# Kernel tuning notes

Measured on AMD Instinct MI355X. Metric: run time of the kernel, lower is better.

Reference implementation:

```python
import jax, jax.numpy as jnp
import numpy as np

D_MODEL = 2048
NUM_HEADS = 16
D_KV = D_MODEL // NUM_HEADS
THETA = 10000.0
N_LORA = 4
RANK = 16
BATCH = 2
SEQ = 2048


def setup_inputs() -> dict:
    key = jax.random.key(0)
    ks = jax.random.split(key, 16)
    s = 0.02
    inp = {
        'x': jax.random.normal(ks[0], (BATCH, SEQ, D_MODEL), jnp.float32),
        'lora_start_indices': jnp.sort(jax.random.randint(ks[1], (N_LORA,), 0, BATCH)),
        'Wq': jax.random.normal(ks[2], (D_MODEL, D_MODEL), jnp.float32) * s,
        'Aq': jax.random.normal(ks[3], (N_LORA, RANK, D_MODEL), jnp.float32) * s,
        'Bq': jax.random.normal(ks[4], (N_LORA, D_MODEL, RANK), jnp.float32) * s,
        'Wk': jax.random.normal(ks[5], (D_MODEL, D_MODEL), jnp.float32) * s,
        'Ak': jax.random.normal(ks[6], (N_LORA, RANK, D_MODEL), jnp.float32) * s,
        'Bk': jax.random.normal(ks[7], (N_LORA, D_MODEL, RANK), jnp.float32) * s,
        'Wv': jax.random.normal(ks[8], (D_MODEL, D_MODEL), jnp.float32) * s,
        'Av': jax.random.normal(ks[9], (N_LORA, RANK, D_MODEL), jnp.float32) * s,
        'Bv': jax.random.normal(ks[10], (N_LORA, D_MODEL, RANK), jnp.float32) * s,
        'Wo': jax.random.normal(ks[11], (D_MODEL, D_MODEL), jnp.float32) * s,
        'Ao': jax.random.normal(ks[12], (N_LORA, RANK, D_MODEL), jnp.float32) * s,
        'Bo': jax.random.normal(ks[13], (N_LORA, D_MODEL, RANK), jnp.float32) * s,
    }
    return inp


def _adapter_ids(starts, batch):
    # each batch row b uses the adapter whose start index is the last one <= b
    ids = jnp.searchsorted(starts, jnp.arange(batch), side='right') - 1
    return jnp.clip(ids, 0, starts.shape[0] - 1)


def _multilora(x, ids, W, A, B):
    # x: [b, s, d_in]; W: [d_out, d_in]; A: [L, r, d_in]; B: [L, d_out, r]
    base = jnp.einsum('bsd,od->bso', x, W)
    Ai, Bi = A[ids], B[ids]                       # [b, r, d_in], [b, d_out, r]
    low = jnp.einsum('bsd,brd->bsr', x, Ai)
    return base + jnp.einsum('bsr,bor->bso', low, Bi)


def _rope(x):
    # x: [b, h, s, d]; interleaved pair rotation
    d = x.shape[-1]
    pos = jnp.arange(x.shape[-2], dtype=jnp.float32)
    inv_freq = THETA ** (-jnp.arange(0, d, 2, dtype=jnp.float32) / d)  # [d/2]
    ang = pos[:, None] * inv_freq[None, :]                              # [s, d/2]
    cos, sin = jnp.cos(ang), jnp.sin(ang)
    x1, x2 = x[..., 0::2], x[..., 1::2]
    o1 = x1 * cos - x2 * sin
    o2 = x1 * sin + x2 * cos
    return jnp.stack([o1, o2], axis=-1).reshape(x.shape)


def reference(x, lora_start_indices, Wq, Aq, Bq, Wk, Ak, Bk, Wv, Av, Bv, Wo, Ao, Bo):
    b, s, _ = x.shape
    ids = _adapter_ids(lora_start_indices, b)
    Q = _multilora(x, ids, Wq, Aq, Bq)
    K = _multilora(x, ids, Wk, Ak, Bk)
    V = _multilora(x, ids, Wv, Av, Bv)
    # [b, s, h*d] -> [b, h, s, d]
    split = lambda t: t.reshape(b, s, NUM_HEADS, D_KV).transpose(0, 2, 1, 3)
    Q, K, V = split(Q), split(K), split(V)
    Q, K = _rope(Q), _rope(K)
    scores = jnp.einsum('bhqd,bhkd->bhqk', Q, K) / jnp.sqrt(jnp.asarray(D_KV, x.dtype))
    causal = jnp.tril(jnp.ones((s, s), bool))
    scores = jnp.where(causal, scores, jnp.asarray(-jnp.inf, scores.dtype))
    attn = jax.nn.softmax(scores, axis=-1)
    out = jnp.einsum('bhqk,bhkd->bhqd', attn, V)
    out = out.transpose(0, 2, 1, 3).reshape(b, s, D_MODEL)
    return _multilora(out, ids, Wo, Ao, Bo)
```

## Files before the change

### kernel.cpp

```cpp
#include <hip/hip_runtime.h>

typedef unsigned short u16;
typedef unsigned int   u32;
typedef __bf16  bf16x8 __attribute__((ext_vector_type(8)));
typedef float   f32x4  __attribute__((ext_vector_type(4)));

#define D_MODEL 2048
#define SEQ     2048
#define NHEAD   16
#define DKV     128
#define RANK    16

__device__ __forceinline__ u16 f2b(float f) {
  union { float f; u32 i; } v; v.f = f;
  u32 i = v.i;
  return (u16)((i + 0x7FFFu + ((i >> 16) & 1u)) >> 16);
}
__device__ __forceinline__ u32 pack2(float lo, float hi) {
  return (u32)f2b(lo) | ((u32)f2b(hi) << 16);
}
__device__ __forceinline__ float b2f(u16 u) {
  union { u32 i; float f; } v; v.i = ((u32)u) << 16; return v.f;
}
__device__ __forceinline__ float dot2(u32 xa, u32 aa) {
  return b2f((u16)(xa & 0xFFFFu)) * b2f((u16)(aa & 0xFFFFu)) +
         b2f((u16)(xa >> 16))     * b2f((u16)(aa >> 16));
}
__device__ __forceinline__ int adapter_id(const int* starts, int b) {
  int cnt = 0;
#pragma unroll
  for (int i = 0; i < 4; ++i) cnt += (starts[i] <= b) ? 1 : 0;
  int id = cnt - 1;
  return id < 0 ? 0 : (id > 3 ? 3 : id);
}
__device__ __forceinline__ f32x4 mfma16(bf16x8 a, bf16x8 b, f32x4 c) {
  return __builtin_amdgcn_mfma_f32_16x16x32_bf16(a, b, c, 0, 0, 0);
}

struct CvtArgs {
  const float* src[13];
  u32 base[14];
};
__global__ __launch_bounds__(256) void convert_kernel(CvtArgs a, u16* __restrict__ dst) {
  const u32 c = blockIdx.x * 256 + threadIdx.x;
  const u32 el0 = c * 8;
  if (el0 >= a.base[13]) return;
  int t = 0;
#pragma unroll
  for (int i = 1; i < 13; ++i) t += (el0 >= a.base[i]) ? 1 : 0;
  const float* s = a.src[t] + (el0 - a.base[t]);
  const float4 lo = *(const float4*)s;
  const float4 hi = *(const float4*)(s + 4);
  uint4 r;
  r.x = pack2(lo.x, lo.y); r.y = pack2(lo.z, lo.w);
  r.z = pack2(hi.x, hi.y); r.w = pack2(hi.z, hi.w);
  *(uint4*)(dst + el0) = r;
}

__global__ __launch_bounds__(256) void lowrank_kernel(
    const u16* __restrict__ X, const u16* __restrict__ A0,
    const u16* __restrict__ A1, const u16* __restrict__ A2,
    const int* __restrict__ starts, float* __restrict__ low, int nout)
{
  const int m = blockIdx.x;
  const int w = threadIdx.x >> 6, lane = threadIdx.x & 63;
  const int id = adapter_id(starts, m >> 11);
  const u16* Xr = X + (size_t)m * D_MODEL;
  for (int o = w; o < nout; o += 4) {
    const int p = o >> 4, r = o & 15;
    const u16* Ar = (p == 0 ? A0 : p == 1 ? A1 : A2) + (size_t)(id * 16 + r) * D_MODEL;
    float sum = 0.f;
#pragma unroll
    for (int c = 0; c < 4; ++c) {
      const int d = c * 512 + lane * 8;
      const uint4 xv = *(const uint4*)(Xr + d);
      const uint4 av = *(const uint4*)(Ar + d);
      sum += dot2(xv.x, av.x) + dot2(xv.y, av.y) + dot2(xv.z, av.z) + dot2(xv.w, av.w);
    }
#pragma unroll
    for (int off = 32; off >= 1; off >>= 1) sum += __shfl_xor(sum, off, 64);
    if (lane == 0) low[(size_t)m * nout + o] = sum;
  }
}

__global__ __launch_bounds__(256, 2) void gemm_kernel(
    const u16* __restrict__ X,
    const u16* __restrict__ W0, const u16* __restrict__ W1, const u16* __restrict__ W2,
    const u16* __restrict__ B0, const u16* __restrict__ B1, const u16* __restrict__ B2,
    const float* __restrict__ low, int ldlow,
    const int* __restrict__ starts,
    u16* __restrict__ D0, u16* __restrict__ D1, u16* __restrict__ D2,
    float* __restrict__ Df, int qkv)
{
  __shared__ __attribute__((aligned(16))) u16 At[128 * 32];
  __shared__ __attribute__((aligned(16))) u16 Bt[128 * 32];
  const int tid = threadIdx.x;
  const int w = tid >> 6, lane = tid & 63, quad = lane >> 4, l16 = lane & 15;
  const int wr = w >> 1, wc = w & 1;
  const int n0 = blockIdx.x * 128, m0 = blockIdx.y * 128, z = blockIdx.z;
  const u16* W  = (z == 0) ? W0 : (z == 1) ? W1 : W2;
  const u16* Bm = (z == 0) ? B0 : (z == 1) ? B1 : B2;
  u16*       D  = (z == 0) ? D0 : (z == 1) ? D1 : D2;
  const int loff = qkv ? z * RANK : 0;
  const int id = adapter_id(starts, m0 >> 11);

  const f32x4 zero4 = {0.f, 0.f, 0.f, 0.f};
  f32x4 acc[4][4];
#pragma unroll
  for (int i = 0; i < 4; ++i)
#pragma unroll
    for (int j = 0; j < 4; ++j) acc[i][j] = zero4;

  const int srow = tid >> 2;
  const int scol = (tid & 3) * 8;
  const u16* Xg = X + (size_t)(m0 + srow) * D_MODEL + scol;
  const u16* Wg = W + (size_t)(n0 + srow) * D_MODEL + scol;

  uint4 ra0 = *(const uint4*)(Xg);
  uint4 ra1 = *(const uint4*)(Xg + 64 * D_MODEL);
  uint4 rb0 = *(const uint4*)(Wg);
  uint4 rb1 = *(const uint4*)(Wg + 64 * D_MODEL);

  for (int kt = 0; kt < D_MODEL / 32; ++kt) {
    *(uint4*)(At + srow * 32 + scol)        = ra0;
    *(uint4*)(At + (64 + srow) * 32 + scol) = ra1;
    *(uint4*)(Bt + srow * 32 + scol)        = rb0;
    *(uint4*)(Bt + (64 + srow) * 32 + scol) = rb1;
    __syncthreads();
    if (kt < D_MODEL / 32 - 1) {
      const int kb = (kt + 1) * 32;
      ra0 = *(const uint4*)(Xg + kb);
      ra1 = *(const uint4*)(Xg + 64 * D_MODEL + kb);
      rb0 = *(const uint4*)(Wg + kb);
      rb1 = *(const uint4*)(Wg + 64 * D_MODEL + kb);
    }
    bf16x8 af[4], bfr[4];
#pragma unroll
    for (int i = 0; i < 4; ++i)
      af[i] = *(const bf16x8*)&At[(wr * 64 + i * 16 + l16) * 32 + quad * 8];
#pragma unroll
    for (int j = 0; j < 4; ++j)
      bfr[j] = *(const bf16x8*)&Bt[(wc * 64 + j * 16 + l16) * 32 + quad * 8];
#pragma unroll
    for (int i = 0; i < 4; ++i)
#pragma unroll
      for (int j = 0; j < 4; ++j)
        acc[i][j] = mfma16(af[i], bfr[j], acc[i][j]);
    __syncthreads();
  }

  for (int e = tid; e < 4096; e += 256) {
    const int rr = e >> 5, kk = e & 31;
    u16 av = 0, bv = 0;
    if (kk < RANK) {
      av = f2b(low[(size_t)(m0 + rr) * ldlow + loff + kk]);
      bv = Bm[((size_t)id * D_MODEL + n0 + rr) * RANK + kk];
    }
    At[rr * 32 + kk] = av;
    Bt[rr * 32 + kk] = bv;
  }
  __syncthreads();
  {
    bf16x8 af[4], bfr[4];
#pragma unroll
    for (int i = 0; i < 4; ++i)
      af[i] = *(const bf16x8*)&At[(wr * 64 + i * 16 + l16) * 32 + quad * 8];
#pragma unroll
    for (int j = 0; j < 4; ++j)
      bfr[j] = *(const bf16x8*)&Bt[(wc * 64 + j * 16 + l16) * 32 + quad * 8];
#pragma unroll
    for (int i = 0; i < 4; ++i)
#pragma unroll
      for (int j = 0; j < 4; ++j)
        acc[i][j] = mfma16(af[i], bfr[j], acc[i][j]);
  }

  const float scale = (qkv && z == 0) ? 0.08838834764831845f : 1.0f;
#pragma unroll
  for (int i = 0; i < 4; ++i) {
    const int mrow = m0 + wr * 64 + i * 16 + quad * 4;
#pragma unroll
    for (int j = 0; j < 4; ++j) {
      const int col = n0 + wc * 64 + j * 16 + l16;
#pragma unroll
      for (int r = 0; r < 4; ++r) {
        const float v = acc[i][j][r] * scale;
        const int m = mrow + r;
        if (qkv) {
          const int bb = m >> 11, s = m & (SEQ - 1);
          const int hh = col >> 7, jj = col & (DKV - 1);
          D[(((size_t)(bb * NHEAD + hh)) * SEQ + s) * DKV + jj] = f2b(v);
        } else {
          Df[(size_t)m * D_MODEL + col] = v;
        }
      }
    }
  }
}

__global__ __launch_bounds__(256) void rope_kernel(u16* __restrict__ Q, u16* __restrict__ K) {
  const u32 idx = blockIdx.x * 256 + threadIdx.x;
  u16* T = (idx & 4194304u) ? K : Q;
  const u32 r  = idx & 4194303u;
  const u32 i  = r & 63u;
  const u32 s  = (r >> 6) & 2047u;
  const u32 bh = r >> 17;
  u16* p = T + ((size_t)bh * SEQ + s) * DKV + 2 * i;
  const u32 v = *(const u32*)p;
  const float x1 = b2f((u16)(v & 0xFFFFu)), x2 = b2f((u16)(v >> 16));
  const float ang = (float)s * exp2f(-0.20762050593046f * (float)i);
  float sn, cs;
  sincosf(ang, &sn, &cs);
  *(u32*)p = pack2(x1 * cs - x2 * sn, x1 * sn + x2 * cs);
}

#define M0 8.0f
__global__ __launch_bounds__(256, 2) void flash_kernel(
    const u16* __restrict__ Q, const u16* __restrict__ K,
    const u16* __restrict__ V, u16* __restrict__ O)
{
  __shared__ __attribute__((aligned(16))) u16 Kl[64 * 136];
  __shared__ __attribute__((aligned(16))) u16 VT[DKV * 72];
  __shared__ __attribute__((aligned(16))) u16 Pl[4 * 16 * 72];
  const int tid = threadIdx.x;
  const int w = tid >> 6, lane = tid & 63, quad = lane >> 4, l16 = lane & 15;
  const int pair = blockIdx.x, bh = blockIdx.y;
  const size_t base = (size_t)bh * SEQ * DKV;
  const u16* Qb = Q + base;
  const u16* Kb = K + base;
  const u16* Vb = V + base;
  const int b = bh >> 4, h = bh & 15;
  u16* Plw = &Pl[w * 1152];
  const f32x4 zero4 = {0.f, 0.f, 0.f, 0.f};

#pragma unroll
  for (int ph = 0; ph < 2; ++ph) {
    const int qt = ph ? (31 - pair) : pair;
    const int q0 = qt * 64;
    bf16x8 qa[4];
#pragma unroll
    for (int kc = 0; kc < 4; ++kc)
      qa[kc] = *(const bf16x8*)(Qb + (size_t)(q0 + w * 16 + l16) * DKV + kc * 32 + quad * 8);
    f32x4 oacc[8];
#pragma unroll
    for (int n = 0; n < 8; ++n) oacc[n] = zero4;
    float lr[4] = {0.f, 0.f, 0.f, 0.f};

    const int nkt = qt + 1;
    for (int kt = 0; kt < nkt; ++kt) {
      __syncthreads();
#pragma unroll
      for (int it = 0; it < 4; ++it) {
        const int c = tid + it * 256;
        const int rr = c >> 4, c8 = (c & 15) * 8;
        *(uint4*)(&Kl[rr * 136 + c8]) = *(const uint4*)(Kb + (size_t)(kt * 64 + rr) * DKV + c8);
      }
#pragma unroll
      for (int it = 0; it < 2; ++it) {
        const int u = tid + it * 256;
        const int rp = u >> 4, c0 = (u & 15) * 8;
        const uint4 a = *(const uint4*)(Vb + (size_t)(kt * 64 + 2 * rp) * DKV + c0);
        const uint4 c = *(const uint4*)(Vb + (size_t)(kt * 64 + 2 * rp + 1) * DKV + c0);
        *(u32*)&VT[(c0 + 0) * 72 + 2 * rp] = (a.x & 0xFFFFu) | (c.x << 16);
        *(u32*)&VT[(c0 + 1) * 72 + 2 * rp] = (a.x >> 16)     | (c.x & 0xFFFF0000u);
        *(u32*)&VT[(c0 + 2) * 72 + 2 * rp] = (a.y & 0xFFFFu) | (c.y << 16);
        *(u32*)&VT[(c0 + 3) * 72 + 2 * rp] = (a.y >> 16)     | (c.y & 0xFFFF0000u);
        *(u32*)&VT[(c0 + 4) * 72 + 2 * rp] = (a.z & 0xFFFFu) | (c.z << 16);
        *(u32*)&VT[(c0 + 5) * 72 + 2 * rp] = (a.z >> 16)     | (c.z & 0xFFFF0000u);
        *(u32*)&VT[(c0 + 6) * 72 + 2 * rp] = (a.w & 0xFFFFu) | (c.w << 16);
        *(u32*)&VT[(c0 + 7) * 72 + 2 * rp] = (a.w >> 16)     | (c.w & 0xFFFF0000u);
      }
      __syncthreads();

      f32x4 sacc[4];
#pragma unroll
      for (int jc = 0; jc < 4; ++jc) sacc[jc] = zero4;
#pragma unroll
      for (int kc = 0; kc < 4; ++kc)
#pragma unroll
        for (int jc = 0; jc < 4; ++jc) {
          const bf16x8 kb = *(const bf16x8*)&Kl[(jc * 16 + l16) * 136 + kc * 32 + quad * 8];
          sacc[jc] = mfma16(qa[kc], kb, sacc[jc]);
        }

      const int last = (kt == nkt - 1);
#pragma unroll
      for (int rg = 0; rg < 4; ++rg) {
        const int qq = q0 + w * 16 + quad * 4 + rg;
        float psum = 0.f;
#pragma unroll
        for (int jc = 0; jc < 4; ++jc) {
          const int kk = kt * 64 + jc * 16 + l16;
          float p = __expf(sacc[jc][rg] - M0);
          if (last && kk > qq) p = 0.f;
          psum += p;
          Plw[(quad * 4 + rg) * 72 + jc * 16 + l16] = f2b(p);
        }
        lr[rg] += psum;
      }

#pragma unroll
      for (int kc = 0; kc < 2; ++kc) {
        const bf16x8 pa = *(const bf16x8*)&Plw[l16 * 72 + kc * 32 + quad * 8];
#pragma unroll
        for (int n = 0; n < 8; ++n) {
          const bf16x8 vb = *(const bf16x8*)&VT[(n * 16 + l16) * 72 + kc * 32 + quad * 8];
          oacc[n] = mfma16(pa, vb, oacc[n]);
        }
      }
    }

#pragma unroll
    for (int rg = 0; rg < 4; ++rg) {
#pragma unroll
      for (int off = 8; off >= 1; off >>= 1) lr[rg] += __shfl_xor(lr[rg], off, 64);
      lr[rg] = 1.f / lr[rg];
    }
#pragma unroll
    for (int n = 0; n < 8; ++n) {
      const int col = h * DKV + n * 16 + l16;
#pragma unroll
      for (int rg = 0; rg < 4; ++rg) {
        const int row = q0 + w * 16 + quad * 4 + rg;
        O[((size_t)b * SEQ + row) * D_MODEL + col] = f2b(oacc[n][rg] * lr[rg]);
      }
    }
  }
}

extern "C" void kernel_launch(void* const* d_in, const int* in_sizes, int n_in,
                              void* d_out, int out_size, void* d_ws, size_t ws_size,
                              hipStream_t stream) {
  (void)in_sizes; (void)n_in; (void)out_size; (void)ws_size;
  const int* starts = (const int*)d_in[1];

  static const u32 XB = 0;
  static const u32 WQ = 8388608, WK = 12582912, WV = 16777216, WO = 20971520;
  static const u32 AQ = 25165824, AK = 25296896, AV = 25427968, AO = 25559040;
  static const u32 BQ = 25690112, BK = 25821184, BV = 25952256, BO = 26083328;
  static const u32 TOT = 26214400;

  u16* wsb = (u16*)d_ws;
  char* ws = (char*)d_ws;
  float* low_qkv = (float*)(ws + 52428800);
  float* low_o   = (float*)(ws + 53215232);
  u16*   Qb      = (u16*)(ws + 53477376);
  u16*   Kb      = (u16*)(ws + 70254592);
  u16*   Vb      = (u16*)(ws + 87031808);
  u16*   attn    = wsb + XB;

  CvtArgs ca;
  ca.src[0]  = (const float*)d_in[0];
  ca.src[1]  = (const float*)d_in[2];
  ca.src[2]  = (const float*)d_in[5];
  ca.src[3]  = (const float*)d_in[8];
  ca.src[4]  = (const float*)d_in[11];
  ca.src[5]  = (const float*)d_in[3];
  ca.src[6]  = (const float*)d_in[6];
  ca.src[7]  = (const float*)d_in[9];
  ca.src[8]  = (const float*)d_in[12];
  ca.src[9]  = (const float*)d_in[4];
  ca.src[10] = (const float*)d_in[7];
  ca.src[11] = (const float*)d_in[10];
  ca.src[12] = (const float*)d_in[13];
  const u32 bases[14] = {XB, WQ, WK, WV, WO, AQ, AK, AV, AO, BQ, BK, BV, BO, TOT};
  for (int i = 0; i < 14; ++i) ca.base[i] = bases[i];

  convert_kernel<<<dim3(TOT / 8 / 256), 256, 0, stream>>>(ca, wsb);

  lowrank_kernel<<<dim3(4096), 256, 0, stream>>>(wsb + XB, wsb + AQ, wsb + AK, wsb + AV,
                                                 starts, low_qkv, 48);
  gemm_kernel<<<dim3(16, 32, 3), 256, 0, stream>>>(
      wsb + XB, wsb + WQ, wsb + WK, wsb + WV, wsb + BQ, wsb + BK, wsb + BV,
      low_qkv, 48, starts, Qb, Kb, Vb, (float*)nullptr, 1);
  rope_kernel<<<dim3(32768), 256, 0, stream>>>(Qb, Kb);
  flash_kernel<<<dim3(16, 32), 256, 0, stream>>>(Qb, Kb, Vb, attn);
  lowrank_kernel<<<dim3(4096), 256, 0, stream>>>(attn, wsb + AO, wsb + AO, wsb + AO,
                                                 starts, low_o, 16);
  gemm_kernel<<<dim3(16, 32, 1), 256, 0, stream>>>(
      attn, wsb + WO, wsb + WO, wsb + WO, wsb + BO, wsb + BO, wsb + BO,
      low_o, 16, starts, (u16*)nullptr, (u16*)nullptr, (u16*)nullptr,
      (float*)d_out, 0);
}
```

Measured before the change: 529.0 us.

## Share K/V tiles across paired query tiles and use direct global-to-LDS loads

The flash kernel now processes both paired query tiles in a single pass over key tiles, so each K/V tile is loaded and transposed into LDS once and reused by both query tiles instead of being loaded twice. The projection GEMM replaces register-staged prefetch with global_load_lds direct copies into shared memory, and RoPE switches to the fast __sincosf intrinsic. Holding two sets of accumulators and Q fragments raises register pressure and may hurt occupancy. Dropping the register prefetch also removes the overlap of global loads with MFMA work in the GEMM, and __sincosf loses accuracy for large angles.

```diff
diff --git a/kernel.cpp b/kernel.cpp
--- a/kernel.cpp
+++ b/kernel.cpp
@@ -35,6 +35,11 @@
 }
 __device__ __forceinline__ f32x4 mfma16(bf16x8 a, bf16x8 b, f32x4 c) {
   return __builtin_amdgcn_mfma_f32_16x16x32_bf16(a, b, c, 0, 0, 0);
+}
+__device__ __forceinline__ void gload16(const u16* g, u16* l) {
+  __builtin_amdgcn_global_load_lds(
+      (const __attribute__((address_space(1))) u32*)(const void*)g,
+      (__attribute__((address_space(3))) u32*)(void*)l, 16, 0, 0);
 }
 
 struct CvtArgs {
@@ -115,25 +120,16 @@
   const int scol = (tid & 3) * 8;
   const u16* Xg = X + (size_t)(m0 + srow) * D_MODEL + scol;
   const u16* Wg = W + (size_t)(n0 + srow) * D_MODEL + scol;
-
-  uint4 ra0 = *(const uint4*)(Xg);
-  uint4 ra1 = *(const uint4*)(Xg + 64 * D_MODEL);
-  uint4 rb0 = *(const uint4*)(Wg);
-  uint4 rb1 = *(const uint4*)(Wg + 64 * D_MODEL);
+  u16* lA = &At[w * 512];
+  u16* lB = &Bt[w * 512];
 
   for (int kt = 0; kt < D_MODEL / 32; ++kt) {
-    *(uint4*)(At + srow * 32 + scol)        = ra0;
-    *(uint4*)(At + (64 + srow) * 32 + scol) = ra1;
-    *(uint4*)(Bt + srow * 32 + scol)        = rb0;
-    *(uint4*)(Bt + (64 + srow) * 32 + scol) = rb1;
+    const int kb = kt * 32;
+    gload16(Xg + kb,                lA);
+    gload16(Xg + 64 * D_MODEL + kb, lA + 2048);
+    gload16(Wg + kb,                lB);
+    gload16(Wg + 64 * D_MODEL + kb, lB + 2048);
     __syncthreads();
-    if (kt < D_MODEL / 32 - 1) {
-      const int kb = (kt + 1) * 32;
-      ra0 = *(const uint4*)(Xg + kb);
-      ra1 = *(const uint4*)(Xg + 64 * D_MODEL + kb);
-      rb0 = *(const uint4*)(Wg + kb);
-      rb1 = *(const uint4*)(Wg + 64 * D_MODEL + kb);
-    }
     bf16x8 af[4], bfr[4];
 #pragma unroll
     for (int i = 0; i < 4; ++i)
@@ -210,7 +206,7 @@
   const float x1 = b2f((u16)(v & 0xFFFFu)), x2 = b2f((u16)(v >> 16));
   const float ang = (float)s * exp2f(-0.20762050593046f * (float)i);
   float sn, cs;
-  sincosf(ang, &sn, &cs);
+  __sincosf(ang, &sn, &cs);
   *(u32*)p = pack2(x1 * cs - x2 * sn, x1 * sn + x2 * cs);
 }
 
@@ -233,97 +229,105 @@
   u16* Plw = &Pl[w * 1152];
   const f32x4 zero4 = {0.f, 0.f, 0.f, 0.f};
 
-#pragma unroll
-  for (int ph = 0; ph < 2; ++ph) {
-    const int qt = ph ? (31 - pair) : pair;
-    const int q0 = qt * 64;
-    bf16x8 qa[4];
+  const int qtA = pair, qtB = 31 - pair;
+  const int q0A = qtA * 64, q0B = qtB * 64;
+
+  bf16x8 qaA[4], qaB[4];
+#pragma unroll
+  for (int kc = 0; kc < 4; ++kc) {
+    qaA[kc] = *(const bf16x8*)(Qb + (size_t)(q0A + w * 16 + l16) * DKV + kc * 32 + quad * 8);
+    qaB[kc] = *(const bf16x8*)(Qb + (size_t)(q0B + w * 16 + l16) * DKV + kc * 32 + quad * 8);
+  }
+  f32x4 oA[8], oB[8];
+#pragma unroll
+  for (int n = 0; n < 8; ++n) { oA[n] = zero4; oB[n] = zero4; }
+  float lrA[4] = {0.f, 0.f, 0.f, 0.f}, lrB[4] = {0.f, 0.f, 0.f, 0.f};
+
+  auto tile = [&](const bf16x8* qa, f32x4* oacc, float* lr, int q0, int kt, int diag) {
+    f32x4 sacc[4];
+#pragma unroll
+    for (int jc = 0; jc < 4; ++jc) sacc[jc] = zero4;
 #pragma unroll
     for (int kc = 0; kc < 4; ++kc)
-      qa[kc] = *(const bf16x8*)(Qb + (size_t)(q0 + w * 16 + l16) * DKV + kc * 32 + quad * 8);
-    f32x4 oacc[8];
-#pragma unroll
-    for (int n = 0; n < 8; ++n) oacc[n] = zero4;
-    float lr[4] = {0.f, 0.f, 0.f, 0.f};
-
-    const int nkt = qt + 1;
-    for (int kt = 0; kt < nkt; ++kt) {
-      __syncthreads();
-#pragma unroll
-      for (int it = 0; it < 4; ++it) {
-        const int c = tid + it * 256;
-        const int rr = c >> 4, c8 = (c & 15) * 8;
-        *(uint4*)(&Kl[rr * 136 + c8]) = *(const uint4*)(Kb + (size_t)(kt * 64 + rr) * DKV + c8);
+#pragma unroll
+      for (int jc = 0; jc < 4; ++jc) {
+        const bf16x8 kb = *(const bf16x8*)&Kl[(jc * 16 + l16) * 136 + kc * 32 + quad * 8];
+        sacc[jc] = mfma16(qa[kc], kb, sacc[jc]);
       }
 #pragma unroll
-      for (int it = 0; it < 2; ++it) {
-        const int u = tid + it * 256;
-        const int rp = u >> 4, c0 = (u & 15) * 8;
-        const uint4 a = *(const uint4*)(Vb + (size_t)(kt * 64 + 2 * rp) * DKV + c0);
-        const uint4 c = *(const uint4*)(Vb + (size_t)(kt * 64 + 2 * rp + 1) * DKV + c0);
-        *(u32*)&VT[(c0 + 0) * 72 + 2 * rp] = (a.x & 0xFFFFu) | (c.x << 16);
-        *(u32*)&VT[(c0 + 1) * 72 + 2 * rp] = (a.x >> 16)     | (c.x & 0xFFFF0000u);
-        *(u32*)&VT[(c0 + 2) * 72 + 2 * rp] = (a.y & 0xFFFFu) | (c.y << 16);
-        *(u32*)&VT[(c0 + 3) * 72 + 2 * rp] = (a.y >> 16)     | (c.y & 0xFFFF0000u);
-        *(u32*)&VT[(c0 + 4) * 72 + 2 * rp] = (a.z & 0xFFFFu) | (c.z << 16);
-        *(u32*)&VT[(c0 + 5) * 72 + 2 * rp] = (a.z >> 16)     | (c.z & 0xFFFF0000u);
-        *(u32*)&VT[(c0 + 6) * 72 + 2 * rp] = (a.w & 0xFFFFu) | (c.w << 16);
-        *(u32*)&VT[(c0 + 7) * 72 + 2 * rp] = (a.w >> 16)     | (c.w & 0xFFFF0000u);
+    for (int rg = 0; rg < 4; ++rg) {
+      const int qq = q0 + w * 16 + quad * 4 + rg;
+      float psum = 0.f;
+#pragma unroll
+      for (int jc = 0; jc < 4; ++jc) {
+        const int kk = kt * 64 + jc * 16 + l16;
+        float p = __expf(sacc[jc][rg] - M0);
+        if (diag && kk > qq) p = 0.f;
+        psum += p;
+        Plw[(quad * 4 + rg) * 72 + jc * 16 + l16] = f2b(p);
       }
-      __syncthreads();
-
-      f32x4 sacc[4];
-#pragma unroll
-      for (int jc = 0; jc < 4; ++jc) sacc[jc] = zero4;
-#pragma unroll
-      for (int kc = 0; kc < 4; ++kc)
-#pragma unroll
-        for (int jc = 0; jc < 4; ++jc) {
-          const bf16x8 kb = *(const bf16x8*)&Kl[(jc * 16 + l16) * 136 + kc * 32 + quad * 8];
-          sacc[jc] = mfma16(qa[kc], kb, sacc[jc]);
-        }
-
-      const int last = (kt == nkt - 1);
-#pragma unroll
-      for (int rg = 0; rg < 4; ++rg) {
-        const int qq = q0 + w * 16 + quad * 4 + rg;
-        float psum = 0.f;
-#pragma unroll
-        for (int jc = 0; jc < 4; ++jc) {
-          const int kk = kt * 64 + jc * 16 + l16;
-          float p = __expf(sacc[jc][rg] - M0);
-          if (last && kk > qq) p = 0.f;
-          psum += p;
-          Plw[(quad * 4 + rg) * 72 + jc * 16 + l16] = f2b(p);
-        }
-        lr[rg] += psum;
+      lr[rg] += psum;
+    }
+#pragma unroll
+    for (int kc = 0; kc < 2; ++kc) {
+      const bf16x8 pa = *(const bf16x8*)&Plw[l16 * 72 + kc * 32 + quad * 8];
+#pragma unroll
+      for (int n = 0; n < 8; ++n) {
+        const bf16x8 vb = *(const bf16x8*)&VT[(n * 16 + l16) * 72 + kc * 32 + quad * 8];
+        oacc[n] = mfma16(pa, vb, oacc[n]);
       }
-
-#pragma unroll
-      for (int kc = 0; kc < 2; ++kc) {
-        const bf16x8 pa = *(const bf16x8*)&Plw[l16 * 72 + kc * 32 + quad * 8];
-#pragma unroll
-        for (int n = 0; n < 8; ++n) {
-          const bf16x8 vb = *(const bf16x8*)&VT[(n * 16 + l16) * 72 + kc * 32 + quad * 8];
-          oacc[n] = mfma16(pa, vb, oacc[n]);
-        }
-      }
-    }
-
+    }
+  };
+
+  const int nkt = qtB + 1;
+  for (int kt = 0; kt < nkt; ++kt) {
+    __syncthreads();
+#pragma unroll
+    for (int it = 0; it < 4; ++it) {
+      const int c = tid + it * 256;
+      const int rr = c >> 4, c8 = (c & 15) * 8;
+      *(uint4*)(&Kl[rr * 136 + c8]) = *(const uint4*)(Kb + (size_t)(kt * 64 + rr) * DKV + c8);
+    }
+#pragma unroll
+    for (int it = 0; it < 2; ++it) {
+      const int u = tid + it * 256;
+      const int rp = u >> 4, c0 = (u & 15) * 8;
+      const uint4 a = *(const uint4*)(Vb + (size_t)(kt * 64 + 2 * rp) * DKV + c0);
+      const uint4 c = *(const uint4*)(Vb + (size_t)(kt * 64 + 2 * rp + 1) * DKV + c0);
+      *(u32*)&VT[(c0 + 0) * 72 + 2 * rp] = (a.x & 0xFFFFu) | (c.x << 16);
+      *(u32*)&VT[(c0 + 1) * 72 + 2 * rp] = (a.x >> 16)     | (c.x & 0xFFFF0000u);
+      *(u32*)&VT[(c0 + 2) * 72 + 2 * rp] = (a.y & 0xFFFFu) | (c.y << 16);
+      *(u32*)&VT[(c0 + 3) * 72 + 2 * rp] = (a.y >> 16)     | (c.y & 0xFFFF0000u);
+      *(u32*)&VT[(c0 + 4) * 72 + 2 * rp] = (a.z & 0xFFFFu) | (c.z << 16);
+      *(u32*)&VT[(c0 + 5) * 72 + 2 * rp] = (a.z >> 16)     | (c.z & 0xFFFF0000u);
+      *(u32*)&VT[(c0 + 6) * 72 + 2 * rp] = (a.w & 0xFFFFu) | (c.w << 16);
+      *(u32*)&VT[(c0 + 7) * 72 + 2 * rp] = (a.w >> 16)     | (c.w & 0xFFFF0000u);
+    }
+    __syncthreads();
+
+    tile(qaB, oB, lrB, q0B, kt, kt == qtB);
+    if (kt <= qtA) tile(qaA, oA, lrA, q0A, kt, kt == qtA);
+  }
+
+#pragma unroll
+  for (int rg = 0; rg < 4; ++rg) {
+#pragma unroll
+    for (int off = 8; off >= 1; off >>= 1) {
+      lrA[rg] += __shfl_xor(lrA[rg], off, 64);
+      lrB[rg] += __shfl_xor(lrB[rg], off, 64);
+    }
+    lrA[rg] = 1.f / lrA[rg];
+    lrB[rg] = 1.f / lrB[rg];
+  }
+#pragma unroll
+  for (int n = 0; n < 8; ++n) {
+    const int col = h * DKV + n * 16 + l16;
 #pragma unroll
     for (int rg = 0; rg < 4; ++rg) {
-#pragma unroll
-      for (int off = 8; off >= 1; off >>= 1) lr[rg] += __shfl_xor(lr[rg], off, 64);
-      lr[rg] = 1.f / lr[rg];
-    }
-#pragma unroll
-    for (int n = 0; n < 8; ++n) {
-      const int col = h * DKV + n * 16 + l16;
-#pragma unroll
-      for (int rg = 0; rg < 4; ++rg) {
-        const int row = q0 + w * 16 + quad * 4 + rg;
-        O[((size_t)b * SEQ + row) * D_MODEL + col] = f2b(oacc[n][rg] * lr[rg]);
-      }
+      const int rowA = q0A + w * 16 + quad * 4 + rg;
+      const int rowB = q0B + w * 16 + quad * 4 + rg;
+      O[((size_t)b * SEQ + rowA) * D_MODEL + col] = f2b(oA[n][rg] * lrA[rg]);
+      O[((size_t)b * SEQ + rowB) * D_MODEL + col] = f2b(oB[n][rg] * lrB[rg]);
     }
   }
 }
```

Result: slower. 580.2 us (+9.7%).

## Split causal attention work evenly across blocks with partial outputs and merge kernel

Applied to the files above, without the earlier changes.

The flash kernel is relaunched with twice as many blocks. Each block processes exactly 16 or 17 KV tiles: short query tiles are finished directly, and the second half of each long tile's KV range is written as an unnormalized partial output plus row sums. A new merge kernel then combines the two partials. The change also software-pipelines K/V global loads into registers one tile ahead, raises the launch bound to 3 blocks per CU, and switches rope to fast __sincosf. The cost is an extra kernel launch and partial-buffer traffic, plus higher register pressure from the prefetch buffers.

```diff
diff --git a/kernel.cpp b/kernel.cpp
--- a/kernel.cpp
+++ b/kernel.cpp
@@ -210,21 +210,22 @@
   const float x1 = b2f((u16)(v & 0xFFFFu)), x2 = b2f((u16)(v >> 16));
   const float ang = (float)s * exp2f(-0.20762050593046f * (float)i);
   float sn, cs;
-  sincosf(ang, &sn, &cs);
+  __sincosf(ang, &sn, &cs);
   *(u32*)p = pack2(x1 * cs - x2 * sn, x1 * sn + x2 * cs);
 }
 
 #define M0 8.0f
-__global__ __launch_bounds__(256, 2) void flash_kernel(
+__global__ __launch_bounds__(256, 3) void flash_kernel(
     const u16* __restrict__ Q, const u16* __restrict__ K,
-    const u16* __restrict__ V, u16* __restrict__ O)
+    const u16* __restrict__ V, u16* __restrict__ O,
+    u16* __restrict__ Opart, float* __restrict__ lpart)
 {
   __shared__ __attribute__((aligned(16))) u16 Kl[64 * 136];
   __shared__ __attribute__((aligned(16))) u16 VT[DKV * 72];
   __shared__ __attribute__((aligned(16))) u16 Pl[4 * 16 * 72];
   const int tid = threadIdx.x;
   const int w = tid >> 6, lane = tid & 63, quad = lane >> 4, l16 = lane & 15;
-  const int pair = blockIdx.x, bh = blockIdx.y;
+  const int cid = blockIdx.x, bh = blockIdx.y;
   const size_t base = (size_t)bh * SEQ * DKV;
   const u16* Qb = Q + base;
   const u16* Kb = K + base;
@@ -233,99 +234,177 @@
   u16* Plw = &Pl[w * 1152];
   const f32x4 zero4 = {0.f, 0.f, 0.f, 0.f};
 
-#pragma unroll
-  for (int ph = 0; ph < 2; ++ph) {
-    const int qt = ph ? (31 - pair) : pair;
-    const int q0 = qt * 64;
-    bf16x8 qa[4];
+  const int dual = (cid < 16);
+  const int nA   = dual ? (cid + 1) : 16;
+  const int qtB  = 31 - cid;
+  const int n    = dual ? 17 : 16;
+
+  const int krr = tid >> 4;
+  const int kc8 = (tid & 15) * 8;
+  const int vrp = tid & 31;
+  const int vcg = tid >> 5;
+
+  int qt = cid, q0 = cid * 64;
+  bf16x8 qa[4];
+#pragma unroll
+  for (int kc = 0; kc < 4; ++kc)
+    qa[kc] = *(const bf16x8*)(Qb + (size_t)(q0 + w * 16 + l16) * DKV + kc * 32 + quad * 8);
+
+  f32x4 oacc[8];
+#pragma unroll
+  for (int nn = 0; nn < 8; ++nn) oacc[nn] = zero4;
+  float lr[4] = {0.f, 0.f, 0.f, 0.f};
+
+  uint4 pk[4], pva[2], pvb[2];
+#pragma unroll
+  for (int it = 0; it < 4; ++it)
+    pk[it] = *(const uint4*)(Kb + (size_t)(krr + it * 16) * DKV + kc8);
+#pragma unroll
+  for (int it = 0; it < 2; ++it) {
+    pva[it] = *(const uint4*)(Vb + (size_t)(2 * vrp)     * DKV + (vcg + it * 8) * 8);
+    pvb[it] = *(const uint4*)(Vb + (size_t)(2 * vrp + 1) * DKV + (vcg + it * 8) * 8);
+  }
+
+  for (int s = 0; s < n; ++s) {
+    if (dual && s == nA) {
+      float inv[4];
+#pragma unroll
+      for (int rg = 0; rg < 4; ++rg) {
+        float t = lr[rg];
+#pragma unroll
+        for (int off = 8; off >= 1; off >>= 1) t += __shfl_xor(t, off, 64);
+        inv[rg] = 1.f / t;
+        lr[rg] = 0.f;
+      }
+#pragma unroll
+      for (int nn = 0; nn < 8; ++nn) {
+        const int col = h * DKV + nn * 16 + l16;
+#pragma unroll
+        for (int rg = 0; rg < 4; ++rg) {
+          const int row = q0 + w * 16 + quad * 4 + rg;
+          O[((size_t)b * SEQ + row) * D_MODEL + col] = f2b(oacc[nn][rg] * inv[rg]);
+        }
+#pragma unroll
+        for (int e = 0; e < 4; ++e) oacc[nn][e] = 0.f;
+      }
+      qt = qtB; q0 = qtB * 64;
+#pragma unroll
+      for (int kc = 0; kc < 4; ++kc)
+        qa[kc] = *(const bf16x8*)(Qb + (size_t)(q0 + w * 16 + l16) * DKV + kc * 32 + quad * 8);
+    }
+    const int kt = (dual && s >= nA) ? (16 + s - nA) : s;
+
+    __syncthreads();
+#pragma unroll
+    for (int it = 0; it < 4; ++it)
+      *(uint4*)(&Kl[(krr + it * 16) * 136 + kc8]) = pk[it];
+#pragma unroll
+    for (int it = 0; it < 2; ++it) {
+      const int c0 = (vcg + it * 8) * 8;
+      const uint4 a = pva[it], c = pvb[it];
+      *(u32*)&VT[(c0 + 0) * 72 + 2 * vrp] = (a.x & 0xFFFFu) | (c.x << 16);
+      *(u32*)&VT[(c0 + 1) * 72 + 2 * vrp] = (a.x >> 16)     | (c.x & 0xFFFF0000u);
+      *(u32*)&VT[(c0 + 2) * 72 + 2 * vrp] = (a.y & 0xFFFFu) | (c.y << 16);
+      *(u32*)&VT[(c0 + 3) * 72 + 2 * vrp] = (a.y >> 16)     | (c.y & 0xFFFF0000u);
+      *(u32*)&VT[(c0 + 4) * 72 + 2 * vrp] = (a.z & 0xFFFFu) | (c.z << 16);
+      *(u32*)&VT[(c0 + 5) * 72 + 2 * vrp] = (a.z >> 16)     | (c.z & 0xFFFF0000u);
+      *(u32*)&VT[(c0 + 6) * 72 + 2 * vrp] = (a.w & 0xFFFFu) | (c.w << 16);
+      *(u32*)&VT[(c0 + 7) * 72 + 2 * vrp] = (a.w >> 16)     | (c.w & 0xFFFF0000u);
+    }
+    __syncthreads();
+
+    if (s + 1 < n) {
+      const int ktn = (dual && (s + 1) >= nA) ? (16 + s + 1 - nA) : (s + 1);
+      const size_t ko = (size_t)ktn * 64 * DKV;
+#pragma unroll
+      for (int it = 0; it < 4; ++it)
+        pk[it] = *(const uint4*)(Kb + ko + (size_t)(krr + it * 16) * DKV + kc8);
+#pragma unroll
+      for (int it = 0; it < 2; ++it) {
+        pva[it] = *(const uint4*)(Vb + ko + (size_t)(2 * vrp)     * DKV + (vcg + it * 8) * 8);
+        pvb[it] = *(const uint4*)(Vb + ko + (size_t)(2 * vrp + 1) * DKV + (vcg + it * 8) * 8);
+      }
+    }
+
+    f32x4 sacc[4];
+#pragma unroll
+    for (int jc = 0; jc < 4; ++jc) sacc[jc] = zero4;
 #pragma unroll
     for (int kc = 0; kc < 4; ++kc)
-      qa[kc] = *(const bf16x8*)(Qb + (size_t)(q0 + w * 16 + l16) * DKV + kc * 32 + quad * 8);
-    f32x4 oacc[8];
-#pragma unroll
-    for (int n = 0; n < 8; ++n) oacc[n] = zero4;
-    float lr[4] = {0.f, 0.f, 0.f, 0.f};
-
-    const int nkt = qt + 1;
-    for (int kt = 0; kt < nkt; ++kt) {
-      __syncthreads();
-#pragma unroll
-      for (int it = 0; it < 4; ++it) {
-        const int c = tid + it * 256;
-        const int rr = c >> 4, c8 = (c & 15) * 8;
-        *(uint4*)(&Kl[rr * 136 + c8]) = *(const uint4*)(Kb + (size_t)(kt * 64 + rr) * DKV + c8);
-      }
-#pragma unroll
-      for (int it = 0; it < 2; ++it) {
-        const int u = tid + it * 256;
-        const int rp = u >> 4, c0 = (u & 15) * 8;
-        const uint4 a = *(const uint4*)(Vb + (size_t)(kt * 64 + 2 * rp) * DKV + c0);
-        const uint4 c = *(const uint4*)(Vb + (size_t)(kt * 64 + 2 * rp + 1) * DKV + c0);
-        *(u32*)&VT[(c0 + 0) * 72 + 2 * rp] = (a.x & 0xFFFFu) | (c.x << 16);
-        *(u32*)&VT[(c0 + 1) * 72 + 2 * rp] = (a.x >> 16)     | (c.x & 0xFFFF0000u);
-        *(u32*)&VT[(c0 + 2) * 72 + 2 * rp] = (a.y & 0xFFFFu) | (c.y << 16);
-        *(u32*)&VT[(c0 + 3) * 72 + 2 * rp] = (a.y >> 16)     | (c.y & 0xFFFF0000u);
-        *(u32*)&VT[(c0 + 4) * 72 + 2 * rp] = (a.z & 0xFFFFu) | (c.z << 16);
-        *(u32*)&VT[(c0 + 5) * 72 + 2 * rp] = (a.z >> 16)     | (c.z & 0xFFFF0000u);
-        *(u32*)&VT[(c0 + 6) * 72 + 2 * rp] = (a.w & 0xFFFFu) | (c.w << 16);
-        *(u32*)&VT[(c0 + 7) * 72 + 2 * rp] = (a.w >> 16)     | (c.w & 0xFFFF0000u);
-      }
-      __syncthreads();
-
-      f32x4 sacc[4];
-#pragma unroll
-      for (int jc = 0; jc < 4; ++jc) sacc[jc] = zero4;
-#pragma unroll
-      for (int kc = 0; kc < 4; ++kc)
-#pragma unroll
-        for (int jc = 0; jc < 4; ++jc) {
-          const bf16x8 kb = *(const bf16x8*)&Kl[(jc * 16 + l16) * 136 + kc * 32 + quad * 8];
-          sacc[jc] = mfma16(qa[kc], kb, sacc[jc]);
-        }
-
-      const int last = (kt == nkt - 1);
-#pragma unroll
-      for (int rg = 0; rg < 4; ++rg) {
-        const int qq = q0 + w * 16 + quad * 4 + rg;
-        float psum = 0.f;
-#pragma unroll
-        for (int jc = 0; jc < 4; ++jc) {
-          const int kk = kt * 64 + jc * 16 + l16;
-          float p = __expf(sacc[jc][rg] - M0);
-          if (last && kk > qq) p = 0.f;
-          psum += p;
-          Plw[(quad * 4 + rg) * 72 + jc * 16 + l16] = f2b(p);
-        }
-        lr[rg] += psum;
-      }
-
-#pragma unroll
-      for (int kc = 0; kc < 2; ++kc) {
-        const bf16x8 pa = *(const bf16x8*)&Plw[l16 * 72 + kc * 32 + quad * 8];
-#pragma unroll
-        for (int n = 0; n < 8; ++n) {
-          const bf16x8 vb = *(const bf16x8*)&VT[(n * 16 + l16) * 72 + kc * 32 + quad * 8];
-          oacc[n] = mfma16(pa, vb, oacc[n]);
-        }
-      }
-    }
-
+#pragma unroll
+      for (int jc = 0; jc < 4; ++jc) {
+        const bf16x8 kb = *(const bf16x8*)&Kl[(jc * 16 + l16) * 136 + kc * 32 + quad * 8];
+        sacc[jc] = mfma16(qa[kc], kb, sacc[jc]);
+      }
+
+    const int diag = (kt == qt);
 #pragma unroll
     for (int rg = 0; rg < 4; ++rg) {
-#pragma unroll
-      for (int off = 8; off >= 1; off >>= 1) lr[rg] += __shfl_xor(lr[rg], off, 64);
-      lr[rg] = 1.f / lr[rg];
-    }
-#pragma unroll
-    for (int n = 0; n < 8; ++n) {
-      const int col = h * DKV + n * 16 + l16;
-#pragma unroll
-      for (int rg = 0; rg < 4; ++rg) {
-        const int row = q0 + w * 16 + quad * 4 + rg;
-        O[((size_t)b * SEQ + row) * D_MODEL + col] = f2b(oacc[n][rg] * lr[rg]);
-      }
-    }
-  }
+      const int qq = q0 + w * 16 + quad * 4 + rg;
+      float psum = 0.f;
+#pragma unroll
+      for (int jc = 0; jc < 4; ++jc) {
+        const int kk = kt * 64 + jc * 16 + l16;
+        float p = __expf(sacc[jc][rg] - M0);
+        if (diag && kk > qq) p = 0.f;
+        psum += p;
+        Plw[(quad * 4 + rg) * 72 + jc * 16 + l16] = f2b(p);
+      }
+      lr[rg] += psum;
+    }
+
+#pragma unroll
+    for (int kc = 0; kc < 2; ++kc) {
+      const bf16x8 pa = *(const bf16x8*)&Plw[l16 * 72 + kc * 32 + quad * 8];
+#pragma unroll
+      for (int nn = 0; nn < 8; ++nn) {
+        const bf16x8 vb = *(const bf16x8*)&VT[(nn * 16 + l16) * 72 + kc * 32 + quad * 8];
+        oacc[nn] = mfma16(pa, vb, oacc[nn]);
+      }
+    }
+  }
+
+  const int j = dual ? 1 : 0;
+  const int slot = (bh * 16 + (qt - 16)) * 2 + j;
+#pragma unroll
+  for (int rg = 0; rg < 4; ++rg) {
+#pragma unroll
+    for (int off = 8; off >= 1; off >>= 1) lr[rg] += __shfl_xor(lr[rg], off, 64);
+  }
+#pragma unroll
+  for (int nn = 0; nn < 8; ++nn) {
+#pragma unroll
+    for (int rg = 0; rg < 4; ++rg) {
+      const int row = w * 16 + quad * 4 + rg;
+      Opart[(size_t)slot * 8192 + row * 128 + nn * 16 + l16] = f2b(oacc[nn][rg]);
+    }
+  }
+  if (l16 == 0) {
+#pragma unroll
+    for (int rg = 0; rg < 4; ++rg)
+      lpart[slot * 64 + w * 16 + quad * 4 + rg] = lr[rg];
+  }
+}
+
+__global__ __launch_bounds__(256) void merge_kernel(
+    const u16* __restrict__ Opart, const float* __restrict__ lpart,
+    u16* __restrict__ O)
+{
+  const u32 t = blockIdx.x * 256 + threadIdx.x;
+  const u32 u   = t & 63;
+  const u32 row = (t >> 6) & 63;
+  const u32 q16 = (t >> 12) & 15;
+  const u32 bh  = t >> 16;
+  const u32 slot0 = (bh * 16 + q16) * 2;
+  const u32 o0 = ((slot0 * 8192u + row * 128u) >> 1) + u;
+  const u32 a = ((const u32*)Opart)[o0];
+  const u32 c = ((const u32*)Opart)[o0 + 4096];
+  const float inv = 1.f / (lpart[slot0 * 64 + row] + lpart[(slot0 + 1) * 64 + row]);
+  const float r0 = (b2f((u16)(a & 0xFFFFu)) + b2f((u16)(c & 0xFFFFu))) * inv;
+  const float r1 = (b2f((u16)(a >> 16))     + b2f((u16)(c >> 16)))     * inv;
+  const u32 bb = bh >> 4, h = bh & 15;
+  const u32 s = (q16 + 16) * 64 + row;
+  ((u32*)O)[(size_t)(bb * SEQ + s) * (D_MODEL / 2) + h * 64 + u] = pack2(r0, r1);
 }
 
 extern "C" void kernel_launch(void* const* d_in, const int* in_sizes, int n_in,
@@ -348,6 +427,8 @@
   u16*   Kb      = (u16*)(ws + 70254592);
   u16*   Vb      = (u16*)(ws + 87031808);
   u16*   attn    = wsb + XB;
+  u16*   Opart   = wsb + WQ;
+  float* lpart   = (float*)(ws + 33554432);
 
   CvtArgs ca;
   ca.src[0]  = (const float*)d_in[0];
@@ -374,7 +455,8 @@
       wsb + XB, wsb + WQ, wsb + WK, wsb + WV, wsb + BQ, wsb + BK, wsb + BV,
       low_qkv, 48, starts, Qb, Kb, Vb, (float*)nullptr, 1);
   rope_kernel<<<dim3(32768), 256, 0, stream>>>(Qb, Kb);
-  flash_kernel<<<dim3(16, 32), 256, 0, stream>>>(Qb, Kb, Vb, attn);
+  flash_kernel<<<dim3(32, 32), 256, 0, stream>>>(Qb, Kb, Vb, attn, Opart, lpart);
+  merge_kernel<<<dim3(8192), 256, 0, stream>>>(Opart, lpart, attn);
   lowrank_kernel<<<dim3(4096), 256, 0, stream>>>(attn, wsb + AO, wsb + AO, wsb + AO,
                                                  starts, low_o, 16);
   gemm_kernel<<<dim3(16, 32, 1), 256, 0, stream>>>(
```

New measurement: 542.9 us. +2.6%, slower.
